# Kernel optimization log

Hardware: AMD Instinct MI355X
Metric: run time of the kernel (lower is better)

Reference implementation:

```python
import jax, jax.numpy as jnp
import numpy as np

B, T, K, D, P, KP = 8, 512, 64, 256, 4, 16
EPS = 1e-6      # weight-denominator eps from __init__
LN_EPS = 1e-5   # torch nn.LayerNorm default


def _ln(x, g, b):
    m = x.mean(-1, keepdims=True)
    var = x.var(-1, keepdims=True)  # biased, matches torch LayerNorm
    return (x - m) * jax.lax.rsqrt(var + LN_EPS) * g + b


def setup_inputs() -> dict:
    key = jax.random.key(0)
    ks = jax.random.split(key, 6)
    E_S = jax.random.normal(ks[0], (B, T, K, D), jnp.float32)
    W = jax.random.uniform(ks[1], (B, T, K), jnp.float32)
    # parts partition the K=64 tokens into P=4 contiguous groups of 16
    part_idx = jnp.arange(P * KP, dtype=jnp.int32).reshape(P, KP)
    part_W = jax.random.normal(ks[2], (P, D, D), jnp.float32) * 0.02   # [P, out, in]
    part_b = jnp.zeros((P, D), jnp.float32)
    v = jax.random.normal(ks[3], (P, D), jnp.float32) * 0.02
    c = jnp.zeros((P,), jnp.float32)
    ln_g = jnp.ones((P, D), jnp.float32)
    ln_b = jnp.zeros((P, D), jnp.float32)
    proj_W = jax.random.normal(ks[4], (D, P * D), jnp.float32) * 0.02  # [out, in]
    proj_b = jnp.zeros((D,), jnp.float32)
    out_g = jnp.ones((D,), jnp.float32)
    out_b = jnp.zeros((D,), jnp.float32)
    return dict(E_S=E_S, W=W, part_idx=part_idx, part_W=part_W, part_b=part_b,
                v=v, c=c, ln_g=ln_g, ln_b=ln_b, proj_W=proj_W, proj_b=proj_b,
                out_g=out_g, out_b=out_b)


def reference(E_S, W, part_idx, part_W, part_b, v, c, ln_g, ln_b,
              proj_W, proj_b, out_g, out_b):
    # gather tokens/weights for all parts at once: [B,T,P,KP,D] / [B,T,P,KP]
    tokens = jnp.take(E_S, part_idx, axis=2)
    w = jnp.take(W, part_idx, axis=2)
    w_norm = w / (w.sum(axis=3, keepdims=True) + EPS)
    # weighted segment-sum over tokens of each part -> [B,T,P,D]
    u = jnp.einsum('btpk,btpkd->btpd', w_norm, tokens)
    # per-part linear (torch Linear: y = x @ W.T + b)
    u_hat = jnp.einsum('btpi,poi->btpo', u, part_W) + part_b
    u_ln = _ln(u_hat, ln_g, ln_b)
    # sigmoid gate per part
    alpha = jax.nn.sigmoid(jnp.einsum('btpd,pd->btp', u_ln, v) + c)
    u_tilde = alpha[..., None] * u_hat
    # concat parts and project
    Z = u_tilde.reshape(B, T, P * D)
    S = Z @ proj_W.T + proj_b
    return _ln(S, out_g, out_b)
```

## Files before the change

kernel.cpp:

```cpp
#include <hip/hip_runtime.h>
#include <hip/hip_bf16.h>

#define ROWS   4096
#define KTOK   64
#define DD     256
#define PP     4
#define EPS_W  1e-6f
#define LN_EPS 1e-5f

typedef __bf16 bf16_t;
typedef __attribute__((ext_vector_type(8))) __bf16 bf16x8;
typedef __attribute__((ext_vector_type(4))) float floatx4;

__device__ __forceinline__ ushort f2bf(float f) {
    union { float f; unsigned int i; } v; v.f = f;
    unsigned int r = v.i + 0x7FFFu + ((v.i >> 16) & 1u);
    return (ushort)(r >> 16);
}

__global__ __launch_bounds__(256) void k_conv(const float* __restrict__ src,
                                              ushort* __restrict__ dst) {
    const int i = (blockIdx.x * 256 + threadIdx.x) * 4;
    float4 a = *reinterpret_cast<const float4*>(&src[i]);
    ushort4 o; o.x = f2bf(a.x); o.y = f2bf(a.y); o.z = f2bf(a.z); o.w = f2bf(a.w);
    *reinterpret_cast<ushort4*>(&dst[i]) = o;
}

__global__ __launch_bounds__(256) void k_u(const float* __restrict__ ES,
                                           const float* __restrict__ Wt,
                                           const int* __restrict__ pidx,
                                           ushort* __restrict__ u_ws) {
    __shared__ float wraw[64], wn[64], denom[4];
    __shared__ int pix[64];
    const int row = blockIdx.x;
    const int tid = threadIdx.x;
    if (tid < 64) {
        pix[tid] = pidx[tid];
        wraw[tid] = Wt[row * 64 + tid];
    }
    __syncthreads();
    if (tid < 4) {
        float s = 0.f;
        for (int j = 0; j < 16; ++j) s += wraw[pix[tid * 16 + j]];
        denom[tid] = s + EPS_W;
    }
    __syncthreads();
    if (tid < 64) wn[tid] = wraw[pix[tid]] / denom[tid >> 4];
    __syncthreads();

    const int p = tid >> 6, l = tid & 63;
    const int d0 = l * 4;
    float a0 = 0.f, a1 = 0.f, a2 = 0.f, a3 = 0.f;
    const size_t rb = (size_t)row * (KTOK * DD);
    for (int j = 0; j < 16; ++j) {
        const int k = pix[p * 16 + j];
        const float wj = wn[p * 16 + j];
        float4 t = *reinterpret_cast<const float4*>(&ES[rb + (size_t)k * DD + d0]);
        a0 += wj * t.x; a1 += wj * t.y;
        a2 += wj * t.z; a3 += wj * t.w;
    }
    ushort4 o; o.x = f2bf(a0); o.y = f2bf(a1); o.z = f2bf(a2); o.w = f2bf(a3);
    *reinterpret_cast<ushort4*>(&u_ws[(size_t)row * 1024 + p * 256 + d0]) = o;
}

__device__ __forceinline__ void gemm_mainloop(const ushort* __restrict__ A, int lda, int acol,
                                              const ushort* __restrict__ Bm, int ldb, int K,
                                              int m0, ushort* ldsA, ushort* ldsB,
                                              floatx4 acc[4][4]) {
    const int tid = threadIdx.x;
    const int w = tid >> 6, l = tid & 63, li = l & 15, quad = l >> 4;
    for (int k0 = 0; k0 < K; k0 += 64) {
        for (int q = tid; q < 512; q += 256) {
            const int r = q >> 3, kc = (q & 7) * 8;
            *reinterpret_cast<uint4*>(&ldsA[r * 64 + kc]) =
                *reinterpret_cast<const uint4*>(&A[(size_t)(m0 + r) * lda + acol + k0 + kc]);
        }
        for (int q = tid; q < 2048; q += 256) {
            const int r = q >> 3, kc = (q & 7) * 8;
            *reinterpret_cast<uint4*>(&ldsB[r * 64 + kc]) =
                *reinterpret_cast<const uint4*>(&Bm[(size_t)r * ldb + k0 + kc]);
        }
        __syncthreads();
        #pragma unroll
        for (int ks = 0; ks < 2; ++ks) {
            bf16x8 af[4], bfm[4];
            #pragma unroll
            for (int mt = 0; mt < 4; ++mt)
                af[mt] = *reinterpret_cast<const bf16x8*>(&ldsA[(mt * 16 + li) * 64 + ks * 32 + quad * 8]);
            #pragma unroll
            for (int nt = 0; nt < 4; ++nt)
                bfm[nt] = *reinterpret_cast<const bf16x8*>(&ldsB[(w * 64 + nt * 16 + li) * 64 + ks * 32 + quad * 8]);
            #pragma unroll
            for (int mt = 0; mt < 4; ++mt)
                #pragma unroll
                for (int nt = 0; nt < 4; ++nt)
                    acc[mt][nt] = __builtin_amdgcn_mfma_f32_16x16x32_bf16(af[mt], bfm[nt], acc[mt][nt], 0, 0, 0);
        }
        __syncthreads();
    }
}

__global__ __launch_bounds__(256) void k_part(const ushort* __restrict__ u_ws,
                                              const ushort* __restrict__ partWb,
                                              const float* __restrict__ part_b,
                                              const float* __restrict__ ln_g,
                                              const float* __restrict__ ln_b,
                                              const float* __restrict__ vv,
                                              const float* __restrict__ cc,
                                              ushort* __restrict__ Z) {
    __shared__ __align__(16) ushort ldsA[64 * 64];
    __shared__ __align__(16) ushort ldsB[256 * 64];
    __shared__ float redbuf[4][64][4];
    __shared__ float alpha_s[64];
    __shared__ float gvred[4][2];
    const int m0 = blockIdx.x * 64;
    const int p = blockIdx.y;
    const int tid = threadIdx.x;
    const int w = tid >> 6, l = tid & 63, li = l & 15, quad = l >> 4;

    {
        const int n = p * 256 + tid;
        float a = ln_g[n] * vv[n];
        float b2 = ln_b[n] * vv[n];
        for (int m = 1; m < 64; m <<= 1) { a += __shfl_xor(a, m, 64); b2 += __shfl_xor(b2, m, 64); }
        if (l == 0) { gvred[w][0] = a; gvred[w][1] = b2; }
    }

    floatx4 acc[4][4];
    #pragma unroll
    for (int mt = 0; mt < 4; ++mt)
        #pragma unroll
        for (int nt = 0; nt < 4; ++nt)
            acc[mt][nt] = (floatx4){0.f, 0.f, 0.f, 0.f};

    gemm_mainloop(u_ws, 1024, p * 256, partWb + (size_t)p * 65536, 256, 256, m0, ldsA, ldsB, acc);

    const float S_gv = gvred[0][0] + gvred[1][0] + gvred[2][0] + gvred[3][0];
    const float S_bv = gvred[0][1] + gvred[1][1] + gvred[2][1] + gvred[3][1];

    float pb[4], gv[4];
    #pragma unroll
    for (int nt = 0; nt < 4; ++nt) {
        const int n = p * 256 + w * 64 + nt * 16 + li;
        pb[nt] = part_b[n];
        gv[nt] = ln_g[n] * vv[n];
    }

    #pragma unroll
    for (int mt = 0; mt < 4; ++mt)
        #pragma unroll
        for (int r = 0; r < 4; ++r) {
            float s1 = 0.f, s2 = 0.f, s3 = 0.f;
            #pragma unroll
            for (int nt = 0; nt < 4; ++nt) {
                float uh = acc[mt][nt][r] + pb[nt];
                acc[mt][nt][r] = uh;
                s1 += uh; s2 += uh * uh; s3 += uh * gv[nt];
            }
            for (int msk = 1; msk < 16; msk <<= 1) {
                s1 += __shfl_xor(s1, msk, 64);
                s2 += __shfl_xor(s2, msk, 64);
                s3 += __shfl_xor(s3, msk, 64);
            }
            if (li == 0) {
                const int rr = mt * 16 + quad * 4 + r;
                redbuf[w][rr][0] = s1; redbuf[w][rr][1] = s2; redbuf[w][rr][2] = s3;
            }
        }
    __syncthreads();
    if (tid < 64) {
        float t1 = 0.f, t2 = 0.f, t3 = 0.f;
        for (int ww = 0; ww < 4; ++ww) {
            t1 += redbuf[ww][tid][0]; t2 += redbuf[ww][tid][1]; t3 += redbuf[ww][tid][2];
        }
        const float mean = t1 * (1.f / 256.f);
        const float var = t2 * (1.f / 256.f) - mean * mean;
        const float rstd = rsqrtf(var + LN_EPS);
        const float arg = rstd * (t3 - mean * S_gv) + S_bv + cc[p];
        alpha_s[tid] = 1.f / (1.f + __expf(-arg));
    }
    __syncthreads();

    #pragma unroll
    for (int mt = 0; mt < 4; ++mt)
        #pragma unroll
        for (int r = 0; r < 4; ++r) {
            const int rr = mt * 16 + quad * 4 + r;
            const float al = alpha_s[rr];
            const size_t rowoff = (size_t)(m0 + rr) * 1024 + p * 256;
            #pragma unroll
            for (int nt = 0; nt < 4; ++nt) {
                const int n = w * 64 + nt * 16 + li;
                Z[rowoff + n] = f2bf(al * acc[mt][nt][r]);
            }
        }
}

__global__ __launch_bounds__(256) void k_proj(const ushort* __restrict__ Zin,
                                              const ushort* __restrict__ projWb,
                                              const float* __restrict__ proj_b,
                                              const float* __restrict__ out_g,
                                              const float* __restrict__ out_b,
                                              float* __restrict__ out) {
    __shared__ __align__(16) ushort ldsA[64 * 64];
    __shared__ __align__(16) ushort ldsB[256 * 64];
    __shared__ float redbuf[4][64][2];
    __shared__ float stats[64][2];
    const int m0 = blockIdx.x * 64;
    const int tid = threadIdx.x;
    const int w = tid >> 6, l = tid & 63, li = l & 15, quad = l >> 4;

    floatx4 acc[4][4];
    #pragma unroll
    for (int mt = 0; mt < 4; ++mt)
        #pragma unroll
        for (int nt = 0; nt < 4; ++nt)
            acc[mt][nt] = (floatx4){0.f, 0.f, 0.f, 0.f};

    gemm_mainloop(Zin, 1024, 0, projWb, 1024, 1024, m0, ldsA, ldsB, acc);

    float pb[4], og[4], ob[4];
    #pragma unroll
    for (int nt = 0; nt < 4; ++nt) {
        const int n = w * 64 + nt * 16 + li;
        pb[nt] = proj_b[n];
        og[nt] = out_g[n];
        ob[nt] = out_b[n];
    }

    #pragma unroll
    for (int mt = 0; mt < 4; ++mt)
        #pragma unroll
        for (int r = 0; r < 4; ++r) {
            float s1 = 0.f, s2 = 0.f;
            #pragma unroll
            for (int nt = 0; nt < 4; ++nt) {
                float uh = acc[mt][nt][r] + pb[nt];
                acc[mt][nt][r] = uh;
                s1 += uh; s2 += uh * uh;
            }
            for (int msk = 1; msk < 16; msk <<= 1) {
                s1 += __shfl_xor(s1, msk, 64);
                s2 += __shfl_xor(s2, msk, 64);
            }
            if (li == 0) {
                const int rr = mt * 16 + quad * 4 + r;
                redbuf[w][rr][0] = s1; redbuf[w][rr][1] = s2;
            }
        }
    __syncthreads();
    if (tid < 64) {
        float t1 = 0.f, t2 = 0.f;
        for (int ww = 0; ww < 4; ++ww) { t1 += redbuf[ww][tid][0]; t2 += redbuf[ww][tid][1]; }
        const float mean = t1 * (1.f / 256.f);
        const float var = t2 * (1.f / 256.f) - mean * mean;
        stats[tid][0] = mean;
        stats[tid][1] = rsqrtf(var + LN_EPS);
    }
    __syncthreads();

    #pragma unroll
    for (int mt = 0; mt < 4; ++mt)
        #pragma unroll
        for (int r = 0; r < 4; ++r) {
            const int rr = mt * 16 + quad * 4 + r;
            const float mean = stats[rr][0], rstd = stats[rr][1];
            const size_t rowoff = (size_t)(m0 + rr) * 256;
            #pragma unroll
            for (int nt = 0; nt < 4; ++nt) {
                const int n = w * 64 + nt * 16 + li;
                out[rowoff + n] = (acc[mt][nt][r] - mean) * rstd * og[nt] + ob[nt];
            }
        }
}

extern "C" void kernel_launch(void* const* d_in, const int* in_sizes, int n_in,
                              void* d_out, int out_size, void* d_ws, size_t ws_size,
                              hipStream_t stream) {
    const float* ES     = (const float*)d_in[0];
    const float* W      = (const float*)d_in[1];
    const int*   pidx   = (const int*)d_in[2];
    const float* partW  = (const float*)d_in[3];
    const float* part_b = (const float*)d_in[4];
    const float* v      = (const float*)d_in[5];
    const float* c      = (const float*)d_in[6];
    const float* ln_g   = (const float*)d_in[7];
    const float* ln_b   = (const float*)d_in[8];
    const float* projW  = (const float*)d_in[9];
    const float* proj_b = (const float*)d_in[10];
    const float* out_g  = (const float*)d_in[11];
    const float* out_b  = (const float*)d_in[12];

    ushort* u_ws   = (ushort*)d_ws;
    ushort* Z      = u_ws + (size_t)ROWS * 1024;
    ushort* partWb = Z + (size_t)ROWS * 1024;
    ushort* projWb = partWb + (size_t)PP * DD * DD;
    float*  out    = (float*)d_out;

    k_conv<<<PP * DD * DD / 1024, 256, 0, stream>>>(partW, partWb);
    k_conv<<<DD * PP * DD / 1024, 256, 0, stream>>>(projW, projWb);
    k_u<<<ROWS, 256, 0, stream>>>(ES, W, pidx, u_ws);
    k_part<<<dim3(ROWS / 64, PP), 256, 0, stream>>>(u_ws, partWb, part_b, ln_g, ln_b, v, c, Z);
    k_proj<<<ROWS / 64, 256, 0, stream>>>(Z, projWb, proj_b, out_g, out_b, out);
}
```

Measured before the change: 458.2 us.

## Fuse pooling into part GEMM, convert weights on the fly, halve proj tile

The weighted token pooling now runs inside the part GEMM kernel and writes the pooled rows straight into a padded LDS A tile, so the u workspace round trip and its kernel launch are gone. The separate weight conversion kernels are also removed: both GEMMs read fp32 weights and convert them to bf16 while staging into LDS, using padded strides to reduce bank conflicts. The projection kernel drops to 32-row tiles, doubling its grid. In exchange, the fp32 weights are reloaded and reconverted by every block, doubling weight traffic per tile, and the pooling phase is serialized before the MFMA loop.

Result: slower. 522.5 us (+14.0%).

```diff
diff --git a/kernel.cpp b/kernel.cpp
--- a/kernel.cpp
+++ b/kernel.cpp
@@ -2,13 +2,9 @@
 #include <hip/hip_bf16.h>
 
 #define ROWS   4096
-#define KTOK   64
-#define DD     256
-#define PP     4
 #define EPS_W  1e-6f
 #define LN_EPS 1e-5f
 
-typedef __bf16 bf16_t;
 typedef __attribute__((ext_vector_type(8))) __bf16 bf16x8;
 typedef __attribute__((ext_vector_type(4))) float floatx4;
 
@@ -18,105 +14,31 @@
     return (ushort)(r >> 16);
 }
 
-__global__ __launch_bounds__(256) void k_conv(const float* __restrict__ src,
-                                              ushort* __restrict__ dst) {
-    const int i = (blockIdx.x * 256 + threadIdx.x) * 4;
-    float4 a = *reinterpret_cast<const float4*>(&src[i]);
-    ushort4 o; o.x = f2bf(a.x); o.y = f2bf(a.y); o.z = f2bf(a.z); o.w = f2bf(a.w);
-    *reinterpret_cast<ushort4*>(&dst[i]) = o;
-}
-
-__global__ __launch_bounds__(256) void k_u(const float* __restrict__ ES,
-                                           const float* __restrict__ Wt,
-                                           const int* __restrict__ pidx,
-                                           ushort* __restrict__ u_ws) {
-    __shared__ float wraw[64], wn[64], denom[4];
-    __shared__ int pix[64];
-    const int row = blockIdx.x;
-    const int tid = threadIdx.x;
-    if (tid < 64) {
-        pix[tid] = pidx[tid];
-        wraw[tid] = Wt[row * 64 + tid];
-    }
-    __syncthreads();
-    if (tid < 4) {
-        float s = 0.f;
-        for (int j = 0; j < 16; ++j) s += wraw[pix[tid * 16 + j]];
-        denom[tid] = s + EPS_W;
-    }
-    __syncthreads();
-    if (tid < 64) wn[tid] = wraw[pix[tid]] / denom[tid >> 4];
-    __syncthreads();
-
-    const int p = tid >> 6, l = tid & 63;
-    const int d0 = l * 4;
-    float a0 = 0.f, a1 = 0.f, a2 = 0.f, a3 = 0.f;
-    const size_t rb = (size_t)row * (KTOK * DD);
-    for (int j = 0; j < 16; ++j) {
-        const int k = pix[p * 16 + j];
-        const float wj = wn[p * 16 + j];
-        float4 t = *reinterpret_cast<const float4*>(&ES[rb + (size_t)k * DD + d0]);
-        a0 += wj * t.x; a1 += wj * t.y;
-        a2 += wj * t.z; a3 += wj * t.w;
-    }
-    ushort4 o; o.x = f2bf(a0); o.y = f2bf(a1); o.z = f2bf(a2); o.w = f2bf(a3);
-    *reinterpret_cast<ushort4*>(&u_ws[(size_t)row * 1024 + p * 256 + d0]) = o;
-}
-
-__device__ __forceinline__ void gemm_mainloop(const ushort* __restrict__ A, int lda, int acol,
-                                              const ushort* __restrict__ Bm, int ldb, int K,
-                                              int m0, ushort* ldsA, ushort* ldsB,
-                                              floatx4 acc[4][4]) {
+__global__ __launch_bounds__(256) void k_pool_part(const float* __restrict__ ES,
+                                                   const float* __restrict__ Wt,
+                                                   const int* __restrict__ pidx,
+                                                   const float* __restrict__ partW,
+                                                   const float* __restrict__ part_b,
+                                                   const float* __restrict__ ln_g,
+                                                   const float* __restrict__ ln_b,
+                                                   const float* __restrict__ vv,
+                                                   const float* __restrict__ cc,
+                                                   ushort* __restrict__ Z) {
+    __shared__ __align__(16) ushort uA[64 * 264];
+    __shared__ __align__(16) ushort ldsB[256 * 72];
+    __shared__ float w_s[64 * 16];
+    __shared__ float wn_s[64 * 16];
+    __shared__ int   pix[16];
+    __shared__ float redbuf[4][64][3];
+    __shared__ float alpha_s[64];
+    __shared__ float gvred[4][2];
+
+    const int m0 = blockIdx.x * 64;
+    const int p  = blockIdx.y;
     const int tid = threadIdx.x;
     const int w = tid >> 6, l = tid & 63, li = l & 15, quad = l >> 4;
-    for (int k0 = 0; k0 < K; k0 += 64) {
-        for (int q = tid; q < 512; q += 256) {
-            const int r = q >> 3, kc = (q & 7) * 8;
-            *reinterpret_cast<uint4*>(&ldsA[r * 64 + kc]) =
-                *reinterpret_cast<const uint4*>(&A[(size_t)(m0 + r) * lda + acol + k0 + kc]);
-        }
-        for (int q = tid; q < 2048; q += 256) {
-            const int r = q >> 3, kc = (q & 7) * 8;
-            *reinterpret_cast<uint4*>(&ldsB[r * 64 + kc]) =
-                *reinterpret_cast<const uint4*>(&Bm[(size_t)r * ldb + k0 + kc]);
-        }
-        __syncthreads();
-        #pragma unroll
-        for (int ks = 0; ks < 2; ++ks) {
-            bf16x8 af[4], bfm[4];
-            #pragma unroll
-            for (int mt = 0; mt < 4; ++mt)
-                af[mt] = *reinterpret_cast<const bf16x8*>(&ldsA[(mt * 16 + li) * 64 + ks * 32 + quad * 8]);
-            #pragma unroll
-            for (int nt = 0; nt < 4; ++nt)
-                bfm[nt] = *reinterpret_cast<const bf16x8*>(&ldsB[(w * 64 + nt * 16 + li) * 64 + ks * 32 + quad * 8]);
-            #pragma unroll
-            for (int mt = 0; mt < 4; ++mt)
-                #pragma unroll
-                for (int nt = 0; nt < 4; ++nt)
-                    acc[mt][nt] = __builtin_amdgcn_mfma_f32_16x16x32_bf16(af[mt], bfm[nt], acc[mt][nt], 0, 0, 0);
-        }
-        __syncthreads();
-    }
-}
-
-__global__ __launch_bounds__(256) void k_part(const ushort* __restrict__ u_ws,
-                                              const ushort* __restrict__ partWb,
-                                              const float* __restrict__ part_b,
-                                              const float* __restrict__ ln_g,
-                                              const float* __restrict__ ln_b,
-                                              const float* __restrict__ vv,
-                                              const float* __restrict__ cc,
-                                              ushort* __restrict__ Z) {
-    __shared__ __align__(16) ushort ldsA[64 * 64];
-    __shared__ __align__(16) ushort ldsB[256 * 64];
-    __shared__ float redbuf[4][64][4];
-    __shared__ float alpha_s[64];
-    __shared__ float gvred[4][2];
-    const int m0 = blockIdx.x * 64;
-    const int p = blockIdx.y;
-    const int tid = threadIdx.x;
-    const int w = tid >> 6, l = tid & 63, li = l & 15, quad = l >> 4;
+
+    if (tid < 16) pix[tid] = pidx[p * 16 + tid];
 
     {
         const int n = p * 256 + tid;
@@ -126,6 +48,38 @@
         if (l == 0) { gvred[w][0] = a; gvred[w][1] = b2; }
     }
 
+    {
+        const int r = tid >> 2, j0 = (tid & 3) * 4;
+        float4 w4 = *reinterpret_cast<const float4*>(&Wt[(size_t)(m0 + r) * 64 + p * 16 + j0]);
+        w_s[r * 16 + j0 + 0] = w4.x; w_s[r * 16 + j0 + 1] = w4.y;
+        w_s[r * 16 + j0 + 2] = w4.z; w_s[r * 16 + j0 + 3] = w4.w;
+    }
+    __syncthreads();
+    if (tid < 64) {
+        float s = 0.f;
+        #pragma unroll
+        for (int j = 0; j < 16; ++j) s += w_s[tid * 16 + j];
+        const float inv = 1.f / (s + EPS_W);
+        #pragma unroll
+        for (int j = 0; j < 16; ++j) wn_s[tid * 16 + j] = w_s[tid * 16 + j] * inv;
+    }
+    __syncthreads();
+
+    for (int rr = 0; rr < 16; ++rr) {
+        const int row = w * 16 + rr;
+        const float* base = ES + ((size_t)(m0 + row) * 64) * 256 + l * 4;
+        float a0 = 0.f, a1 = 0.f, a2 = 0.f, a3 = 0.f;
+        #pragma unroll
+        for (int j = 0; j < 16; ++j) {
+            const int tk = pix[j];
+            const float wj = wn_s[row * 16 + j];
+            float4 t = *reinterpret_cast<const float4*>(base + (size_t)tk * 256);
+            a0 += wj * t.x; a1 += wj * t.y; a2 += wj * t.z; a3 += wj * t.w;
+        }
+        ushort4 o; o.x = f2bf(a0); o.y = f2bf(a1); o.z = f2bf(a2); o.w = f2bf(a3);
+        *reinterpret_cast<ushort4*>(&uA[row * 264 + l * 4]) = o;
+    }
+
     floatx4 acc[4][4];
     #pragma unroll
     for (int mt = 0; mt < 4; ++mt)
@@ -133,7 +87,34 @@
         for (int nt = 0; nt < 4; ++nt)
             acc[mt][nt] = (floatx4){0.f, 0.f, 0.f, 0.f};
 
-    gemm_mainloop(u_ws, 1024, p * 256, partWb + (size_t)p * 65536, 256, 256, m0, ldsA, ldsB, acc);
+    const float* Bsrc = partW + (size_t)p * 65536;
+    for (int k0 = 0; k0 < 256; k0 += 64) {
+        __syncthreads();
+        #pragma unroll
+        for (int i = 0; i < 16; ++i) {
+            const int q = tid + i * 256;
+            const int n = q >> 4, kc = (q & 15) * 4;
+            float4 b4 = *reinterpret_cast<const float4*>(&Bsrc[(size_t)n * 256 + k0 + kc]);
+            ushort4 o; o.x = f2bf(b4.x); o.y = f2bf(b4.y); o.z = f2bf(b4.z); o.w = f2bf(b4.w);
+            *reinterpret_cast<ushort4*>(&ldsB[n * 72 + kc]) = o;
+        }
+        __syncthreads();
+        #pragma unroll
+        for (int ks = 0; ks < 2; ++ks) {
+            bf16x8 af[4], bfm[4];
+            #pragma unroll
+            for (int mt = 0; mt < 4; ++mt)
+                af[mt] = *reinterpret_cast<const bf16x8*>(&uA[(mt * 16 + li) * 264 + k0 + ks * 32 + quad * 8]);
+            #pragma unroll
+            for (int nt = 0; nt < 4; ++nt)
+                bfm[nt] = *reinterpret_cast<const bf16x8*>(&ldsB[(w * 64 + nt * 16 + li) * 72 + ks * 32 + quad * 8]);
+            #pragma unroll
+            for (int mt = 0; mt < 4; ++mt)
+                #pragma unroll
+                for (int nt = 0; nt < 4; ++nt)
+                    acc[mt][nt] = __builtin_amdgcn_mfma_f32_16x16x32_bf16(af[mt], bfm[nt], acc[mt][nt], 0, 0, 0);
+        }
+    }
 
     const float S_gv = gvred[0][0] + gvred[1][0] + gvred[2][0] + gvred[3][0];
     const float S_bv = gvred[0][1] + gvred[1][1] + gvred[2][1] + gvred[3][1];
@@ -197,27 +178,58 @@
 }
 
 __global__ __launch_bounds__(256) void k_proj(const ushort* __restrict__ Zin,
-                                              const ushort* __restrict__ projWb,
+                                              const float* __restrict__ projW,
                                               const float* __restrict__ proj_b,
                                               const float* __restrict__ out_g,
                                               const float* __restrict__ out_b,
                                               float* __restrict__ out) {
-    __shared__ __align__(16) ushort ldsA[64 * 64];
-    __shared__ __align__(16) ushort ldsB[256 * 64];
-    __shared__ float redbuf[4][64][2];
-    __shared__ float stats[64][2];
-    const int m0 = blockIdx.x * 64;
+    __shared__ __align__(16) ushort ldsA[32 * 72];
+    __shared__ __align__(16) ushort ldsB[256 * 72];
+    __shared__ float redbuf[4][32][2];
+    __shared__ float stats[32][2];
+    const int m0 = blockIdx.x * 32;
     const int tid = threadIdx.x;
     const int w = tid >> 6, l = tid & 63, li = l & 15, quad = l >> 4;
 
-    floatx4 acc[4][4];
-    #pragma unroll
-    for (int mt = 0; mt < 4; ++mt)
+    floatx4 acc[2][4];
+    #pragma unroll
+    for (int mt = 0; mt < 2; ++mt)
         #pragma unroll
         for (int nt = 0; nt < 4; ++nt)
             acc[mt][nt] = (floatx4){0.f, 0.f, 0.f, 0.f};
 
-    gemm_mainloop(Zin, 1024, 0, projWb, 1024, 1024, m0, ldsA, ldsB, acc);
+    for (int k0 = 0; k0 < 1024; k0 += 64) {
+        __syncthreads();
+        {
+            const int r = tid >> 3, kc = (tid & 7) * 8;
+            *reinterpret_cast<uint4*>(&ldsA[r * 72 + kc]) =
+                *reinterpret_cast<const uint4*>(&Zin[(size_t)(m0 + r) * 1024 + k0 + kc]);
+        }
+        #pragma unroll
+        for (int i = 0; i < 16; ++i) {
+            const int q = tid + i * 256;
+            const int n = q >> 4, kc = (q & 15) * 4;
+            float4 b4 = *reinterpret_cast<const float4*>(&projW[(size_t)n * 1024 + k0 + kc]);
+            ushort4 o; o.x = f2bf(b4.x); o.y = f2bf(b4.y); o.z = f2bf(b4.z); o.w = f2bf(b4.w);
+            *reinterpret_cast<ushort4*>(&ldsB[n * 72 + kc]) = o;
+        }
+        __syncthreads();
+        #pragma unroll
+        for (int ks = 0; ks < 2; ++ks) {
+            bf16x8 af[2], bfm[4];
+            #pragma unroll
+            for (int mt = 0; mt < 2; ++mt)
+                af[mt] = *reinterpret_cast<const bf16x8*>(&ldsA[(mt * 16 + li) * 72 + ks * 32 + quad * 8]);
+            #pragma unroll
+            for (int nt = 0; nt < 4; ++nt)
+                bfm[nt] = *reinterpret_cast<const bf16x8*>(&ldsB[(w * 64 + nt * 16 + li) * 72 + ks * 32 + quad * 8]);
+            #pragma unroll
+            for (int mt = 0; mt < 2; ++mt)
+                #pragma unroll
+                for (int nt = 0; nt < 4; ++nt)
+                    acc[mt][nt] = __builtin_amdgcn_mfma_f32_16x16x32_bf16(af[mt], bfm[nt], acc[mt][nt], 0, 0, 0);
+        }
+    }
 
     float pb[4], og[4], ob[4];
     #pragma unroll
@@ -229,7 +241,7 @@
     }
 
     #pragma unroll
-    for (int mt = 0; mt < 4; ++mt)
+    for (int mt = 0; mt < 2; ++mt)
         #pragma unroll
         for (int r = 0; r < 4; ++r) {
             float s1 = 0.f, s2 = 0.f;
@@ -249,7 +261,7 @@
             }
         }
     __syncthreads();
-    if (tid < 64) {
+    if (tid < 32) {
         float t1 = 0.f, t2 = 0.f;
         for (int ww = 0; ww < 4; ++ww) { t1 += redbuf[ww][tid][0]; t2 += redbuf[ww][tid][1]; }
         const float mean = t1 * (1.f / 256.f);
@@ -260,7 +272,7 @@
     __syncthreads();
 
     #pragma unroll
-    for (int mt = 0; mt < 4; ++mt)
+    for (int mt = 0; mt < 2; ++mt)
         #pragma unroll
         for (int r = 0; r < 4; ++r) {
             const int rr = mt * 16 + quad * 4 + r;
@@ -291,15 +303,10 @@
     const float* out_g  = (const float*)d_in[11];
     const float* out_b  = (const float*)d_in[12];
 
-    ushort* u_ws   = (ushort*)d_ws;
-    ushort* Z      = u_ws + (size_t)ROWS * 1024;
-    ushort* partWb = Z + (size_t)ROWS * 1024;
-    ushort* projWb = partWb + (size_t)PP * DD * DD;
-    float*  out    = (float*)d_out;
-
-    k_conv<<<PP * DD * DD / 1024, 256, 0, stream>>>(partW, partWb);
-    k_conv<<<DD * PP * DD / 1024, 256, 0, stream>>>(projW, projWb);
-    k_u<<<ROWS, 256, 0, stream>>>(ES, W, pidx, u_ws);
-    k_part<<<dim3(ROWS / 64, PP), 256, 0, stream>>>(u_ws, partWb, part_b, ln_g, ln_b, v, c, Z);
-    k_proj<<<ROWS / 64, 256, 0, stream>>>(Z, projWb, proj_b, out_g, out_b, out);
+    ushort* Z   = (ushort*)d_ws;
+    float*  out = (float*)d_out;
+
+    k_pool_part<<<dim3(ROWS / 64, 4), 256, 0, stream>>>(ES, W, pidx, partW, part_b,
+                                                        ln_g, ln_b, v, c, Z);
+    k_proj<<<ROWS / 32, 256, 0, stream>>>(Z, projW, proj_b, out_g, out_b, out);
 }
```

## Shrink projection tile to 16 rows, pad LDS rows, merge conversion launches

Applied to the files above, without the earlier changes.

The output projection GEMM now uses 16-row tiles, giving four times as many workgroups so more compute units are busy, at the cost of re-reading the projection weights more often. LDS tiles in both GEMMs are padded to a stride of 72 to reduce bank conflicts. The two weight-conversion launches are merged into one kernel, and the token-sum loop is unrolled. The shared GEMM helper is inlined into each kernel.

New measurement: 413.4 us. 9.8% less time.

```diff
diff --git a/kernel.cpp b/kernel.cpp
--- a/kernel.cpp
+++ b/kernel.cpp
@@ -2,13 +2,9 @@
 #include <hip/hip_bf16.h>
 
 #define ROWS   4096
-#define KTOK   64
-#define DD     256
-#define PP     4
 #define EPS_W  1e-6f
 #define LN_EPS 1e-5f
 
-typedef __bf16 bf16_t;
 typedef __attribute__((ext_vector_type(8))) __bf16 bf16x8;
 typedef __attribute__((ext_vector_type(4))) float floatx4;
 
@@ -18,9 +14,14 @@
     return (ushort)(r >> 16);
 }
 
-__global__ __launch_bounds__(256) void k_conv(const float* __restrict__ src,
-                                              ushort* __restrict__ dst) {
-    const int i = (blockIdx.x * 256 + threadIdx.x) * 4;
+__global__ __launch_bounds__(256) void k_conv(const float* __restrict__ partW,
+                                              const float* __restrict__ projW,
+                                              ushort* __restrict__ partWb,
+                                              ushort* __restrict__ projWb) {
+    const float* src; ushort* dst; int base;
+    if (blockIdx.x < 256) { src = partW; dst = partWb; base = blockIdx.x * 1024; }
+    else                  { src = projW; dst = projWb; base = (blockIdx.x - 256) * 1024; }
+    const int i = base + threadIdx.x * 4;
     float4 a = *reinterpret_cast<const float4*>(&src[i]);
     ushort4 o; o.x = f2bf(a.x); o.y = f2bf(a.y); o.z = f2bf(a.z); o.w = f2bf(a.w);
     *reinterpret_cast<ushort4*>(&dst[i]) = o;
@@ -51,53 +52,17 @@
     const int p = tid >> 6, l = tid & 63;
     const int d0 = l * 4;
     float a0 = 0.f, a1 = 0.f, a2 = 0.f, a3 = 0.f;
-    const size_t rb = (size_t)row * (KTOK * DD);
+    const size_t rb = (size_t)row * (64 * 256);
+    #pragma unroll
     for (int j = 0; j < 16; ++j) {
         const int k = pix[p * 16 + j];
         const float wj = wn[p * 16 + j];
-        float4 t = *reinterpret_cast<const float4*>(&ES[rb + (size_t)k * DD + d0]);
+        float4 t = *reinterpret_cast<const float4*>(&ES[rb + (size_t)k * 256 + d0]);
         a0 += wj * t.x; a1 += wj * t.y;
         a2 += wj * t.z; a3 += wj * t.w;
     }
     ushort4 o; o.x = f2bf(a0); o.y = f2bf(a1); o.z = f2bf(a2); o.w = f2bf(a3);
     *reinterpret_cast<ushort4*>(&u_ws[(size_t)row * 1024 + p * 256 + d0]) = o;
-}
-
-__device__ __forceinline__ void gemm_mainloop(const ushort* __restrict__ A, int lda, int acol,
-                                              const ushort* __restrict__ Bm, int ldb, int K,
-                                              int m0, ushort* ldsA, ushort* ldsB,
-                                              floatx4 acc[4][4]) {
-    const int tid = threadIdx.x;
-    const int w = tid >> 6, l = tid & 63, li = l & 15, quad = l >> 4;
-    for (int k0 = 0; k0 < K; k0 += 64) {
-        for (int q = tid; q < 512; q += 256) {
-            const int r = q >> 3, kc = (q & 7) * 8;
-            *reinterpret_cast<uint4*>(&ldsA[r * 64 + kc]) =
-                *reinterpret_cast<const uint4*>(&A[(size_t)(m0 + r) * lda + acol + k0 + kc]);
-        }
-        for (int q = tid; q < 2048; q += 256) {
-            const int r = q >> 3, kc = (q & 7) * 8;
-            *reinterpret_cast<uint4*>(&ldsB[r * 64 + kc]) =
-                *reinterpret_cast<const uint4*>(&Bm[(size_t)r * ldb + k0 + kc]);
-        }
-        __syncthreads();
-        #pragma unroll
-        for (int ks = 0; ks < 2; ++ks) {
-            bf16x8 af[4], bfm[4];
-            #pragma unroll
-            for (int mt = 0; mt < 4; ++mt)
-                af[mt] = *reinterpret_cast<const bf16x8*>(&ldsA[(mt * 16 + li) * 64 + ks * 32 + quad * 8]);
-            #pragma unroll
-            for (int nt = 0; nt < 4; ++nt)
-                bfm[nt] = *reinterpret_cast<const bf16x8*>(&ldsB[(w * 64 + nt * 16 + li) * 64 + ks * 32 + quad * 8]);
-            #pragma unroll
-            for (int mt = 0; mt < 4; ++mt)
-                #pragma unroll
-                for (int nt = 0; nt < 4; ++nt)
-                    acc[mt][nt] = __builtin_amdgcn_mfma_f32_16x16x32_bf16(af[mt], bfm[nt], acc[mt][nt], 0, 0, 0);
-        }
-        __syncthreads();
-    }
 }
 
 __global__ __launch_bounds__(256) void k_part(const ushort* __restrict__ u_ws,
@@ -108,9 +73,9 @@
                                               const float* __restrict__ vv,
                                               const float* __restrict__ cc,
                                               ushort* __restrict__ Z) {
-    __shared__ __align__(16) ushort ldsA[64 * 64];
-    __shared__ __align__(16) ushort ldsB[256 * 64];
-    __shared__ float redbuf[4][64][4];
+    __shared__ __align__(16) ushort ldsA[64 * 72];
+    __shared__ __align__(16) ushort ldsB[256 * 72];
+    __shared__ float redbuf[4][64][3];
     __shared__ float alpha_s[64];
     __shared__ float gvred[4][2];
     const int m0 = blockIdx.x * 64;
@@ -133,7 +98,40 @@
         for (int nt = 0; nt < 4; ++nt)
             acc[mt][nt] = (floatx4){0.f, 0.f, 0.f, 0.f};
 
-    gemm_mainloop(u_ws, 1024, p * 256, partWb + (size_t)p * 65536, 256, 256, m0, ldsA, ldsB, acc);
+    const ushort* Bsrc = partWb + (size_t)p * 65536;
+    for (int k0 = 0; k0 < 256; k0 += 64) {
+        __syncthreads();
+        #pragma unroll
+        for (int i = 0; i < 2; ++i) {
+            const int q = tid + i * 256;
+            const int r = q >> 3, kc = (q & 7) * 8;
+            *reinterpret_cast<uint4*>(&ldsA[r * 72 + kc]) =
+                *reinterpret_cast<const uint4*>(&u_ws[(size_t)(m0 + r) * 1024 + p * 256 + k0 + kc]);
+        }
+        #pragma unroll
+        for (int i = 0; i < 8; ++i) {
+            const int q = tid + i * 256;
+            const int n = q >> 3, kc = (q & 7) * 8;
+            *reinterpret_cast<uint4*>(&ldsB[n * 72 + kc]) =
+                *reinterpret_cast<const uint4*>(&Bsrc[(size_t)n * 256 + k0 + kc]);
+        }
+        __syncthreads();
+        #pragma unroll
+        for (int ks = 0; ks < 2; ++ks) {
+            bf16x8 af[4], bfm[4];
+            #pragma unroll
+            for (int mt = 0; mt < 4; ++mt)
+                af[mt] = *reinterpret_cast<const bf16x8*>(&ldsA[(mt * 16 + li) * 72 + ks * 32 + quad * 8]);
+            #pragma unroll
+            for (int nt = 0; nt < 4; ++nt)
+                bfm[nt] = *reinterpret_cast<const bf16x8*>(&ldsB[(w * 64 + nt * 16 + li) * 72 + ks * 32 + quad * 8]);
+            #pragma unroll
+            for (int mt = 0; mt < 4; ++mt)
+                #pragma unroll
+                for (int nt = 0; nt < 4; ++nt)
+                    acc[mt][nt] = __builtin_amdgcn_mfma_f32_16x16x32_bf16(af[mt], bfm[nt], acc[mt][nt], 0, 0, 0);
+        }
+    }
 
     const float S_gv = gvred[0][0] + gvred[1][0] + gvred[2][0] + gvred[3][0];
     const float S_bv = gvred[0][1] + gvred[1][1] + gvred[2][1] + gvred[3][1];
@@ -202,22 +200,46 @@
                                               const float* __restrict__ out_g,
                                               const float* __restrict__ out_b,
                                               float* __restrict__ out) {
-    __shared__ __align__(16) ushort ldsA[64 * 64];
-    __shared__ __align__(16) ushort ldsB[256 * 64];
-    __shared__ float redbuf[4][64][2];
-    __shared__ float stats[64][2];
-    const int m0 = blockIdx.x * 64;
+    __shared__ __align__(16) ushort ldsA[16 * 72];
+    __shared__ __align__(16) ushort ldsB[256 * 72];
+    __shared__ float redbuf[4][16][2];
+    __shared__ float stats[16][2];
+    const int m0 = blockIdx.x * 16;
     const int tid = threadIdx.x;
     const int w = tid >> 6, l = tid & 63, li = l & 15, quad = l >> 4;
 
-    floatx4 acc[4][4];
-    #pragma unroll
-    for (int mt = 0; mt < 4; ++mt)
-        #pragma unroll
-        for (int nt = 0; nt < 4; ++nt)
-            acc[mt][nt] = (floatx4){0.f, 0.f, 0.f, 0.f};
-
-    gemm_mainloop(Zin, 1024, 0, projWb, 1024, 1024, m0, ldsA, ldsB, acc);
+    floatx4 acc[4];
+    #pragma unroll
+    for (int nt = 0; nt < 4; ++nt)
+        acc[nt] = (floatx4){0.f, 0.f, 0.f, 0.f};
+
+    for (int k0 = 0; k0 < 1024; k0 += 64) {
+        __syncthreads();
+        if (tid < 128) {
+            const int r = tid >> 3, kc = (tid & 7) * 8;
+            *reinterpret_cast<uint4*>(&ldsA[r * 72 + kc]) =
+                *reinterpret_cast<const uint4*>(&Zin[(size_t)(m0 + r) * 1024 + k0 + kc]);
+        }
+        #pragma unroll
+        for (int i = 0; i < 8; ++i) {
+            const int q = tid + i * 256;
+            const int n = q >> 3, kc = (q & 7) * 8;
+            *reinterpret_cast<uint4*>(&ldsB[n * 72 + kc]) =
+                *reinterpret_cast<const uint4*>(&projWb[(size_t)n * 1024 + k0 + kc]);
+        }
+        __syncthreads();
+        #pragma unroll
+        for (int ks = 0; ks < 2; ++ks) {
+            bf16x8 af, bfm[4];
+            af = *reinterpret_cast<const bf16x8*>(&ldsA[li * 72 + ks * 32 + quad * 8]);
+            #pragma unroll
+            for (int nt = 0; nt < 4; ++nt)
+                bfm[nt] = *reinterpret_cast<const bf16x8*>(&ldsB[(w * 64 + nt * 16 + li) * 72 + ks * 32 + quad * 8]);
+            #pragma unroll
+            for (int nt = 0; nt < 4; ++nt)
+                acc[nt] = __builtin_amdgcn_mfma_f32_16x16x32_bf16(af, bfm[nt], acc[nt], 0, 0, 0);
+        }
+    }
 
     float pb[4], og[4], ob[4];
     #pragma unroll
@@ -229,27 +251,25 @@
     }
 
     #pragma unroll
-    for (int mt = 0; mt < 4; ++mt)
-        #pragma unroll
-        for (int r = 0; r < 4; ++r) {
-            float s1 = 0.f, s2 = 0.f;
-            #pragma unroll
-            for (int nt = 0; nt < 4; ++nt) {
-                float uh = acc[mt][nt][r] + pb[nt];
-                acc[mt][nt][r] = uh;
-                s1 += uh; s2 += uh * uh;
-            }
-            for (int msk = 1; msk < 16; msk <<= 1) {
-                s1 += __shfl_xor(s1, msk, 64);
-                s2 += __shfl_xor(s2, msk, 64);
-            }
-            if (li == 0) {
-                const int rr = mt * 16 + quad * 4 + r;
-                redbuf[w][rr][0] = s1; redbuf[w][rr][1] = s2;
-            }
-        }
-    __syncthreads();
-    if (tid < 64) {
+    for (int r = 0; r < 4; ++r) {
+        float s1 = 0.f, s2 = 0.f;
+        #pragma unroll
+        for (int nt = 0; nt < 4; ++nt) {
+            float uh = acc[nt][r] + pb[nt];
+            acc[nt][r] = uh;
+            s1 += uh; s2 += uh * uh;
+        }
+        for (int msk = 1; msk < 16; msk <<= 1) {
+            s1 += __shfl_xor(s1, msk, 64);
+            s2 += __shfl_xor(s2, msk, 64);
+        }
+        if (li == 0) {
+            const int rr = quad * 4 + r;
+            redbuf[w][rr][0] = s1; redbuf[w][rr][1] = s2;
+        }
+    }
+    __syncthreads();
+    if (tid < 16) {
         float t1 = 0.f, t2 = 0.f;
         for (int ww = 0; ww < 4; ++ww) { t1 += redbuf[ww][tid][0]; t2 += redbuf[ww][tid][1]; }
         const float mean = t1 * (1.f / 256.f);
@@ -260,18 +280,16 @@
     __syncthreads();
 
     #pragma unroll
-    for (int mt = 0; mt < 4; ++mt)
-        #pragma unroll
-        for (int r = 0; r < 4; ++r) {
-            const int rr = mt * 16 + quad * 4 + r;
-            const float mean = stats[rr][0], rstd = stats[rr][1];
-            const size_t rowoff = (size_t)(m0 + rr) * 256;
-            #pragma unroll
-            for (int nt = 0; nt < 4; ++nt) {
-                const int n = w * 64 + nt * 16 + li;
-                out[rowoff + n] = (acc[mt][nt][r] - mean) * rstd * og[nt] + ob[nt];
-            }
-        }
+    for (int r = 0; r < 4; ++r) {
+        const int rr = quad * 4 + r;
+        const float mean = stats[rr][0], rstd = stats[rr][1];
+        const size_t rowoff = (size_t)(m0 + rr) * 256;
+        #pragma unroll
+        for (int nt = 0; nt < 4; ++nt) {
+            const int n = w * 64 + nt * 16 + li;
+            out[rowoff + n] = (acc[nt][r] - mean) * rstd * og[nt] + ob[nt];
+        }
+    }
 }
 
 extern "C" void kernel_launch(void* const* d_in, const int* in_sizes, int n_in,
@@ -294,12 +312,11 @@
     ushort* u_ws   = (ushort*)d_ws;
     ushort* Z      = u_ws + (size_t)ROWS * 1024;
     ushort* partWb = Z + (size_t)ROWS * 1024;
-    ushort* projWb = partWb + (size_t)PP * DD * DD;
+    ushort* projWb = partWb + 262144;
     float*  out    = (float*)d_out;
 
-    k_conv<<<PP * DD * DD / 1024, 256, 0, stream>>>(partW, partWb);
-    k_conv<<<DD * PP * DD / 1024, 256, 0, stream>>>(projW, projWb);
+    k_conv<<<512, 256, 0, stream>>>(partW, projW, partWb, projWb);
     k_u<<<ROWS, 256, 0, stream>>>(ES, W, pidx, u_ws);
-    k_part<<<dim3(ROWS / 64, PP), 256, 0, stream>>>(u_ws, partWb, part_b, ln_g, ln_b, v, c, Z);
-    k_proj<<<ROWS / 64, 256, 0, stream>>>(Z, projWb, proj_b, out_g, out_b, out);
-}
+    k_part<<<dim3(ROWS / 64, 4), 256, 0, stream>>>(u_ws, partWb, part_b, ln_g, ln_b, v, c, Z);
+    k_proj<<<ROWS / 16, 256, 0, stream>>>(Z, projWb, proj_b, out_g, out_b, out);
+}
```
